# Kernel optimization log

Hardware: AMD Instinct MI355X
Metric: run time of the kernel (lower is better)

The kernel has to match this reference:

```python
import jax, jax.numpy as jnp
import numpy as np

N_NODES = 100000
N_EDGES = 1600000
HIDDEN = 64
N_LAYERS = 3
N_CLASSES = 2
N_GRAPHS = 128
NEG_SLOPE = 0.2  # PyG GATConv default negative_slope


def setup_inputs() -> dict:
    key = jax.random.key(0)
    ks = jax.random.split(key, 8)
    x = jax.random.randint(ks[0], (N_NODES,), 0, 2)
    edge_index = jax.random.randint(ks[1], (2, N_EDGES), 0, N_NODES)
    batch = jnp.sort(jax.random.randint(ks[2], (N_NODES,), 0, N_GRAPHS))
    scale = 1.0 / np.sqrt(HIDDEN)
    embed_table = jax.random.normal(ks[3], (2, HIDDEN), jnp.float32)
    Ws = jax.random.normal(ks[4], (N_LAYERS, HIDDEN, HIDDEN), jnp.float32) * scale
    a_srcs = jax.random.normal(ks[5], (N_LAYERS, HIDDEN), jnp.float32) * scale
    a_dsts = jax.random.normal(ks[6], (N_LAYERS, HIDDEN), jnp.float32) * scale
    biases = jnp.zeros((N_LAYERS, HIDDEN), jnp.float32)
    W_out = jax.random.normal(ks[7], (HIDDEN, N_CLASSES), jnp.float32) * scale
    b_out = jnp.zeros((N_CLASSES,), jnp.float32)
    return {"x": x, "edge_index": edge_index, "batch": batch,
            "embed_table": embed_table, "Ws": Ws, "a_srcs": a_srcs,
            "a_dsts": a_dsts, "biases": biases, "W_out": W_out, "b_out": b_out}


def _gat_layer(h, src, dst, W, a_s, a_d, b):
    # h: [N, D]; src/dst: [E'] (self loops included) -> PyG GATConv, heads=1
    hW = h @ W                                   # [N, D]
    e = jax.nn.leaky_relu((hW @ a_s)[src] + (hW @ a_d)[dst], NEG_SLOPE)  # [E']
    m = jax.ops.segment_max(e, dst, num_segments=N_NODES)               # stable softmax per dst
    ex = jnp.exp(e - m[dst])
    denom = jax.ops.segment_sum(ex, dst, num_segments=N_NODES)
    alpha = ex / denom[dst]                      # [E']
    out = jax.ops.segment_sum(hW[src] * alpha[:, None], dst, num_segments=N_NODES)
    return out + b


def reference(x, edge_index, batch, embed_table, Ws, a_srcs, a_dsts, biases, W_out, b_out):
    loop = jnp.arange(N_NODES)
    src = jnp.concatenate([edge_index[0], loop])  # PyG add_self_loops=True
    dst = jnp.concatenate([edge_index[1], loop])
    h = embed_table[x]                            # [N, D]
    for l in range(N_LAYERS):
        h = _gat_layer(h, src, dst, Ws[l], a_srcs[l], a_dsts[l], biases[l])
        if l < N_LAYERS - 1:
            h = jax.nn.relu(h)
    sums = jax.ops.segment_sum(h, batch, num_segments=N_GRAPHS)
    counts = jax.ops.segment_sum(jnp.ones((N_NODES,), h.dtype), batch, num_segments=N_GRAPHS)
    pooled = sums / jnp.maximum(counts, 1.0)[:, None]  # global_mean_pool
    return pooled @ W_out + b_out                      # [G, num_classes]
```

## Files before the change

### kernel.cpp

```cpp
#include <hip/hip_runtime.h>
#include <hip/hip_bf16.h>
#include <float.h>

#define N_NODES 100000
#define N_EDGES 1600000
#define HIDDEN 64
#define N_GRAPHS 128
#define NEG_SLOPE 0.2f
#define ETOT (N_EDGES + N_NODES)

#define BSHIFT 9
#define NB ((N_NODES + 511) >> BSHIFT)
#define PAIR_CHUNK 4096
#define PAIR_BLOCKS ((N_EDGES + PAIR_CHUNK - 1) / PAIR_CHUNK)
#define XBIT_BLOCKS ((N_NODES + 255) / 256)
#define TBL_BLOCKS (NLVL / 4)

#define NREP 64
#define REP_STRIDE 272
#define NLVL 512

__device__ __forceinline__ unsigned short f2bf(float f) {
    unsigned u = __float_as_uint(f);
    unsigned r = (u + 0x7FFFu + ((u >> 16) & 1u)) >> 16;
    return (unsigned short)r;
}
__device__ __forceinline__ float blo(unsigned u) { return __uint_as_float(u << 16); }
__device__ __forceinline__ float bhi(unsigned u) { return __uint_as_float(u & 0xFFFF0000u); }
__device__ __forceinline__ int sb0(unsigned u) { return (int)((unsigned)(u << 24)) >> 24; }
__device__ __forceinline__ int sb1(unsigned u) { return (int)((unsigned)(u << 16)) >> 24; }
__device__ __forceinline__ int sb2(unsigned u) { return (int)((unsigned)(u << 8)) >> 24; }
__device__ __forceinline__ int sb3(unsigned u) { return (int)u >> 24; }


__global__ __launch_bounds__(256) void k_prep(
    const int* __restrict__ e1, const int* __restrict__ x,
    const float* __restrict__ embed, const float* __restrict__ Ws,
    const float* __restrict__ biases, const float* __restrict__ a_srcs,
    const float* __restrict__ a_dsts, const float* __restrict__ W_out,
    int* __restrict__ blockcnt, float* __restrict__ pool_acc,
    unsigned* __restrict__ xb,
    unsigned char* __restrict__ Tq8, float* __restrict__ Tscl,
    float* __restrict__ Ts1s, float* __restrict__ Ts1d,
    float* __restrict__ sparams)
{
    __shared__ int hcnt[NB];
    int t = threadIdx.x, b = blockIdx.x;

    if (b < PAIR_BLOCKS) {
        if (t < NB) hcnt[t] = 0;
        if (b < NREP && t < 2 * N_GRAPHS) pool_acc[b * REP_STRIDE + t] = 0.f;
        __syncthreads();
        int ebase = b * PAIR_CHUNK;
        int ecount = min(PAIR_CHUNK, N_EDGES - ebase);
        for (int i = t; i < ecount; i += 256)
            atomicAdd(&hcnt[e1[ebase + i] >> BSHIFT], 1);
        __syncthreads();
        if (t < NB) blockcnt[b * NB + t] = hcnt[t];
    } else if (b < PAIR_BLOCKS + TBL_BLOCKS) {
        int l = (b - PAIR_BLOCKS) * 4 + (t >> 6);
        int f = t & 63;
        float r0 = 0.f, r1 = 0.f;
#pragma unroll 8
        for (int k = 0; k < 64; ++k) {
            float w = Ws[k * 64 + f];
            r0 = fmaf(embed[k], w, r0);
            r1 = fmaf(embed[64 + k], w, r1);
        }
        if (l == 0) {
            float as = a_srcs[f], ad = a_dsts[f];
            float t0 = r0 * as, t1 = r1 * as, t2 = r0 * ad, t3 = r1 * ad;
#pragma unroll
            for (int off = 32; off >= 1; off >>= 1) {
                t0 += __shfl_xor(t0, off); t1 += __shfl_xor(t1, off);
                t2 += __shfl_xor(t2, off); t3 += __shfl_xor(t3, off);
            }
            if (f == 0) { sparams[0] = t0; sparams[1] = t1; sparams[2] = t2; sparams[3] = t3; }
        }
        if (l == 1) {
            float b2 = biases[128 + f];
            float t4 = b2 * W_out[f * 2];
            float t5 = b2 * W_out[f * 2 + 1];
#pragma unroll
            for (int off = 32; off >= 1; off >>= 1) {
                t4 += __shfl_xor(t4, off); t5 += __shfl_xor(t5, off);
            }
            if (f == 0) { sparams[4] = t4; sparams[5] = t5; }
        }
        float c1 = (float)l * (1.f / (NLVL - 1));
        float o = fmaxf(biases[f] + r0 + c1 * (r1 - r0), 0.f);
        const float* W1 = Ws + 4096;
        float h = 0.f;
#pragma unroll 8
        for (int k = 0; k < 64; ++k) h = fmaf(__shfl(o, k), W1[k * 64 + f], h);
        float ss = h * a_srcs[64 + f];
        float sd = h * a_dsts[64 + f];
        float am = fabsf(h);
#pragma unroll
        for (int off = 32; off >= 1; off >>= 1) {
            ss += __shfl_xor(ss, off);
            sd += __shfl_xor(sd, off);
            am = fmaxf(am, __shfl_xor(am, off));
        }
        float iscl = (am > 0.f) ? 127.f / am : 0.f;
        Tq8[l * 64 + f] = (unsigned char)(__float2int_rn(h * iscl) & 255);
        if (f == 0) { Tscl[l] = am * (1.f / 127.f); Ts1s[l] = ss; Ts1d[l] = sd; }
    } else {
        int i = (b - PAIR_BLOCKS - TBL_BLOCKS) * 256 + t;
        int lane = t & 63;
        bool bb = (i < N_NODES) && (x[i] != 0);
        unsigned long long m = __ballot(bb);
        int wid = i >> 6;
        if (i < N_NODES + 64) {
            if (lane == 0) xb[wid * 2] = (unsigned)m;
            if (lane == 32) xb[wid * 2 + 1] = (unsigned)(m >> 32);
        }
    }
}

__global__ __launch_bounds__(64) void k_scan_bases(int* __restrict__ blockcnt,
                                                   int* __restrict__ btot) {
    int b = blockIdx.x;
    int lane = threadIdx.x;
    int s = 0;
    for (int base = 0; base < PAIR_BLOCKS; base += 64) {
        int c = base + lane;
        int v = (c < PAIR_BLOCKS) ? blockcnt[c * NB + b] : 0;
        int xv = v;
#pragma unroll
        for (int off = 1; off < 64; off <<= 1) {
            int y = __shfl_up(xv, off);
            if (lane >= off) xv += y;
        }
        if (c < PAIR_BLOCKS) blockcnt[c * NB + b] = s + xv - v;
        s += __shfl(xv, 63);
    }
    if (lane == 0) btot[b] = s;
}

__global__ __launch_bounds__(256) void k_pair_scatter(
    const int* __restrict__ e0, const int* __restrict__ e1,
    const unsigned* __restrict__ xb, const int* __restrict__ btot,
    const int* __restrict__ blockcnt, int* __restrict__ pairs)
{
    __shared__ int tot[256];
    __shared__ int cnt[NB];
    __shared__ int base[NB];
    int t = threadIdx.x, b = blockIdx.x;
    int v = (t < NB) ? btot[t] : 0;
    tot[t] = v;
    __syncthreads();
    for (int off = 1; off < 256; off <<= 1) {
        int u = (t >= off) ? tot[t - off] : 0;
        __syncthreads();
        tot[t] += u;
        __syncthreads();
    }
    if (t < NB) {
        cnt[t] = 0;
        base[t] = (tot[t] - v) + blockcnt[b * NB + t];
    }
    __syncthreads();
    int ebase = b * PAIR_CHUNK;
    int ecount = min(PAIR_CHUNK, N_EDGES - ebase);
    for (int i = t; i < ecount; i += 256) {
        int s = e0[ebase + i];
        int d = e1[ebase + i];
        int xv = (xb[s >> 5] >> (s & 31)) & 1;
        int B = d >> BSHIFT;
        int idx = atomicAdd(&cnt[B], 1);
        pairs[base[B] + idx] = (xv << 26) | ((d & 511) << 17) | s;
    }
}

__global__ __launch_bounds__(512) void k_csr_bucket(
    const int* __restrict__ pairs, const int* __restrict__ btot,
    const int* __restrict__ x, const float* __restrict__ sparams,
    int* __restrict__ rowptr, int* __restrict__ col,
    unsigned short* __restrict__ cidx)
{
    __shared__ int deg[512];
    __shared__ int excl[512];
    __shared__ int cnt2[512];
    __shared__ int wsum[8];
    __shared__ int p0sh;
    int b = blockIdx.x;
    int t = threadIdx.x;
    int nb = b << BSHIFT;
    int nodes = min(512, N_NODES - nb);

    int pv = (t < b) ? btot[t] : 0;
#pragma unroll
    for (int off = 32; off >= 1; off >>= 1) pv += __shfl_xor(pv, off);
    if ((t & 63) == 0) wsum[t >> 6] = pv;
    __syncthreads();
    if (t == 0) {
        int s = 0;
#pragma unroll
        for (int i = 0; i < 8; ++i) s += wsum[i];
        p0sh = s;
    }

    int xself = (t < nodes) ? (x[nb + t] & 1) : 0;
    deg[t] = (t < nodes) ? (1 | (xself << 16)) : 0;
    cnt2[t] = 1;
    __syncthreads();
    int p0 = p0sh;
    int p1 = p0 + btot[b];
    for (int i = p0 + t; i < p1; i += 512) {
        int p = pairs[i];
        atomicAdd(&deg[(p >> 17) & 511], 1 | (((p >> 26) & 1) << 16));
    }
    __syncthreads();

    int packed = deg[t];
    int val = packed & 0xFFFF;
    int kx = packed >> 16;
    if (t < nodes) {
        float ss0 = sparams[0], ss1 = sparams[1];
        float sd = xself ? sparams[3] : sparams[2];
        float e0 = ss0 + sd; e0 = (e0 >= 0.f) ? e0 : NEG_SLOPE * e0;
        float e1 = ss1 + sd; e1 = (e1 >= 0.f) ? e1 : NEG_SLOPE * e1;
        float pp0 = __expf(e0), pp1 = __expf(e1);
        float kn = (float)kx, dn = (float)(val - kx);
        float c1 = kn * pp1 / (dn * pp0 + kn * pp1);
        cidx[nb + t] = (unsigned short)__float2int_rn(c1 * (float)(NLVL - 1));
    }

    int xx = val;
#pragma unroll
    for (int off = 1; off < 64; off <<= 1) {
        int y = __shfl_up(xx, off);
        if ((t & 63) >= off) xx += y;
    }
    __syncthreads();
    if ((t & 63) == 63) wsum[t >> 6] = xx;
    __syncthreads();
    if (t == 0) {
        int s = 0;
#pragma unroll
        for (int i = 0; i < 8; ++i) { int v = wsum[i]; wsum[i] = s; s += v; }
    }
    __syncthreads();
    int ex = xx - val + wsum[t >> 6];
    excl[t] = ex;

    int colbase = p0 + nb;
    if (t < nodes) {
        rowptr[nb + t] = colbase + ex;
        col[colbase + ex] = nb + t;
    }
    if (b == NB - 1 && t == 0) rowptr[N_NODES] = ETOT;
    __syncthreads();
    for (int i = p0 + t; i < p1; i += 512) {
        int p = pairs[i];
        int li = (p >> 17) & 511;
        int pos = colbase + excl[li] + atomicAdd(&cnt2[li], 1);
        col[pos] = p & 0x1FFFF;
    }
}


__global__ __launch_bounds__(256) void k_agg1(
    const unsigned char* __restrict__ Tq8, const float* __restrict__ Tscl,
    const float* __restrict__ Ts1s, const float* __restrict__ Ts1d,
    const unsigned short* __restrict__ cidx, const int* __restrict__ col,
    const int* __restrict__ rowptr, const float* __restrict__ bias,
    unsigned short* __restrict__ hout)
{
    __shared__ float2 stash[4][64];
    int t = threadIdx.x;
    int wave = t >> 6, lane = t & 63;
    int h = lane >> 5, hl = lane & 31;
    int base = blockIdx.x * 8 + wave * 2;
    if (base >= N_NODES) return;
    const char* hb = (const char*)Tq8;

    int node = base + h;
    bool valid = (node < N_NODES);
    int row = 0, end = 0;
    if (valid) { row = rowptr[node]; end = rowptr[node + 1]; }
    int deg = end - row;
    int degO = __shfl_xor(deg, 32);
    bool fast = (deg <= 32) && (degO <= 32);

    if (fast) {
        int idx = 0;
        float p = 0.f, sc = 0.f;
        if (hl < deg) idx = cidx[col[row + hl]];
        float sdi = Ts1d[__shfl(idx, h * 32)];
        if (hl < deg) {
            float ee = Ts1s[idx] + sdi;
            ee = (ee >= 0.f) ? ee : NEG_SLOPE * ee;
            p = __expf(ee);
            sc = Tscl[idx];
        }
        stash[wave][lane] = make_float2(p * sc, __int_as_float(idx * 64));

        int q = hl >> 4;
        int f = hl & 15;
        int f4 = f * 4;
        int sb = h * 32;
        float a0 = 0.f, a1 = 0.f, a2 = 0.f, a3 = 0.f;
        int degr = (deg + 7) & ~7;
        for (int j = q; j < degr; j += 8) {
            float2 e0 = stash[wave][sb + j];
            float2 e1 = stash[wave][sb + j + 2];
            float2 e2 = stash[wave][sb + j + 4];
            float2 e3 = stash[wave][sb + j + 6];
            unsigned v0 = *(const unsigned*)(hb + (__float_as_int(e0.y) + f4));
            unsigned v1 = *(const unsigned*)(hb + (__float_as_int(e1.y) + f4));
            unsigned v2 = *(const unsigned*)(hb + (__float_as_int(e2.y) + f4));
            unsigned v3 = *(const unsigned*)(hb + (__float_as_int(e3.y) + f4));
            a0 = fmaf(e0.x, (float)sb0(v0), a0);
            a1 = fmaf(e0.x, (float)sb1(v0), a1);
            a2 = fmaf(e0.x, (float)sb2(v0), a2);
            a3 = fmaf(e0.x, (float)sb3(v0), a3);
            a0 = fmaf(e1.x, (float)sb0(v1), a0);
            a1 = fmaf(e1.x, (float)sb1(v1), a1);
            a2 = fmaf(e1.x, (float)sb2(v1), a2);
            a3 = fmaf(e1.x, (float)sb3(v1), a3);
            a0 = fmaf(e2.x, (float)sb0(v2), a0);
            a1 = fmaf(e2.x, (float)sb1(v2), a1);
            a2 = fmaf(e2.x, (float)sb2(v2), a2);
            a3 = fmaf(e2.x, (float)sb3(v2), a3);
            a0 = fmaf(e3.x, (float)sb0(v3), a0);
            a1 = fmaf(e3.x, (float)sb1(v3), a1);
            a2 = fmaf(e3.x, (float)sb2(v3), a2);
            a3 = fmaf(e3.x, (float)sb3(v3), a3);
        }
        float denom = p;
#pragma unroll
        for (int off = 16; off >= 1; off >>= 1) denom += __shfl_xor(denom, off);
        float inv = 1.f / denom;
        a0 += __shfl_xor(a0, 16);
        a1 += __shfl_xor(a1, 16);
        a2 += __shfl_xor(a2, 16);
        a3 += __shfl_xor(a3, 16);
        if (hl < 16 && valid) {
            float4 bb = *(const float4*)&bias[4 * f];
            ushort4 pk;
            pk.x = f2bf(fmaxf(fmaf(a0, inv, bb.x), 0.f));
            pk.y = f2bf(fmaxf(fmaf(a1, inv, bb.y), 0.f));
            pk.z = f2bf(fmaxf(fmaf(a2, inv, bb.z), 0.f));
            pk.w = f2bf(fmaxf(fmaf(a3, inv, bb.w), 0.f));
            *(ushort4*)&hout[node * 64 + 4 * f] = pk;
        }
    } else {
        for (int s = 0; s < 2; ++s) {
            int nd = base + s;
            if (nd >= N_NODES) continue;
            int r = rowptr[nd], e = rowptr[nd + 1];
            float sdi = Ts1d[cidx[nd]];
            float m = -FLT_MAX;
            for (int j = r + lane; j < e; j += 64) {
                float ee = Ts1s[cidx[col[j]]] + sdi;
                ee = (ee >= 0.f) ? ee : NEG_SLOPE * ee;
                m = fmaxf(m, ee);
            }
#pragma unroll
            for (int off = 32; off >= 1; off >>= 1) m = fmaxf(m, __shfl_xor(m, off));
            float denom = 0.f;
            for (int j = r + lane; j < e; j += 64) {
                float ee = Ts1s[cidx[col[j]]] + sdi;
                ee = (ee >= 0.f) ? ee : NEG_SLOPE * ee;
                denom += __expf(ee - m);
            }
#pragma unroll
            for (int off = 32; off >= 1; off >>= 1) denom += __shfl_xor(denom, off);
            float inv = 1.f / denom;
            float acc = 0.f;
            for (int j = r; j < e; ++j) {
                int idxj = cidx[col[j]];
                float ee = Ts1s[idxj] + sdi;
                ee = (ee >= 0.f) ? ee : NEG_SLOPE * ee;
                float w = __expf(ee - m) * inv * Tscl[idxj];
                int bq = (int)(signed char)Tq8[idxj * 64 + lane];
                acc = fmaf(w, (float)bq, acc);
            }
            hout[nd * 64 + lane] = f2bf(fmaxf(acc + bias[lane], 0.f));
        }
    }
}


__global__ __launch_bounds__(256) void k_gemm2(
    const unsigned* __restrict__ h32, const float* __restrict__ W,
    const float* __restrict__ a_s, const float* __restrict__ a_d,
    const float* __restrict__ W_out,
    float2* __restrict__ z2, float* __restrict__ s_src, float* __restrict__ s_dst)
{
    __shared__ float Wl[64 * 64];
    __shared__ float hT[64 * 68];
    int t = threadIdx.x;
    int r0 = blockIdx.x * 64;

    for (int i = t; i < 4096; i += 256) Wl[i] = W[i];
    for (int i = t; i < 2048; i += 256) {
        int r = i >> 5, m = i & 31;
        int row = r0 + r;
        unsigned u = (row < N_NODES) ? h32[row * 32 + m] : 0u;
        hT[(2 * m) * 68 + r]     = blo(u);
        hT[(2 * m + 1) * 68 + r] = bhi(u);
    }
    __syncthreads();

    int tcol = t & 15;
    int trow = t >> 4;
    float acc[4][4];
#pragma unroll
    for (int i = 0; i < 4; ++i)
#pragma unroll
        for (int j = 0; j < 4; ++j) acc[i][j] = 0.f;

    for (int k = 0; k < 64; ++k) {
        float4 va = *(const float4*)&hT[k * 68 + trow * 4];
        float4 vb = *(const float4*)&Wl[k * 64 + tcol * 4];
        float a[4] = {va.x, va.y, va.z, va.w};
        float bb[4] = {vb.x, vb.y, vb.z, vb.w};
#pragma unroll
        for (int i = 0; i < 4; ++i)
#pragma unroll
            for (int j = 0; j < 4; ++j) acc[i][j] = fmaf(a[i], bb[j], acc[i][j]);
    }

    float4 as4 = *(const float4*)&a_s[tcol * 4];
    float4 ad4 = *(const float4*)&a_d[tcol * 4];
    float asr[4] = {as4.x, as4.y, as4.z, as4.w};
    float adr[4] = {ad4.x, ad4.y, ad4.z, ad4.w};
    float4 wa = *(const float4*)&W_out[8 * tcol];
    float4 wb = *(const float4*)&W_out[8 * tcol + 4];

#pragma unroll
    for (int i = 0; i < 4; ++i) {
        int row = r0 + trow * 4 + i;
        float ps = 0.f, pd = 0.f;
#pragma unroll
        for (int j = 0; j < 4; ++j) {
            ps = fmaf(acc[i][j], asr[j], ps);
            pd = fmaf(acc[i][j], adr[j], pd);
        }
        float z0 = acc[i][0] * wa.x + acc[i][1] * wa.z + acc[i][2] * wb.x + acc[i][3] * wb.z;
        float z1 = acc[i][0] * wa.y + acc[i][1] * wa.w + acc[i][2] * wb.y + acc[i][3] * wb.w;
#pragma unroll
        for (int off = 8; off >= 1; off >>= 1) {
            ps += __shfl_xor(ps, off);
            pd += __shfl_xor(pd, off);
            z0 += __shfl_xor(z0, off);
            z1 += __shfl_xor(z1, off);
        }
        if (row < N_NODES && tcol == 0) {
            s_src[row] = ps; s_dst[row] = pd;
            z2[row] = make_float2(z0, z1);
        }
    }
}


__global__ __launch_bounds__(256) void k_pool2(
    const float2* __restrict__ z2, const int* __restrict__ col,
    const int* __restrict__ rowptr, const float* __restrict__ s_src_in,
    const float* __restrict__ s_dst_in, const int* __restrict__ batch,
    float* __restrict__ pool_acc)
{
    int t = threadIdx.x;
    int wave = t >> 6, lane = t & 63;
    int h = lane >> 5, hl = lane & 31;
    int base0 = blockIdx.x * 32 + wave * 8;
    if (base0 >= N_NODES) return;
    float* rep = pool_acc + ((blockIdx.x * 4 + wave) & (NREP - 1)) * REP_STRIDE;

    int gcur = -1;
    float acc0 = 0.f, acc1 = 0.f;

#pragma unroll
    for (int i = 0; i < 4; ++i) {
        int node = base0 + 2 * i + h;
        bool valid = (node < N_NODES);
        int row = 0, end = 0;
        if (valid) { row = rowptr[node]; end = rowptr[node + 1]; }
        int deg = end - row;
        int degO = __shfl_xor(deg, 32);
        bool fast = (deg <= 32) && (degO <= 32);
        float r0 = 0.f, r1 = 0.f;

        if (fast) {
            float sdi = valid ? s_dst_in[node] : 0.f;
            float p = 0.f;
            float2 zv = make_float2(0.f, 0.f);
            if (hl < deg) {
                int c = col[row + hl];
                float ee = s_src_in[c] + sdi;
                ee = (ee >= 0.f) ? ee : NEG_SLOPE * ee;
                p = __expf(ee);
                zv = z2[c];
            }
            float n0 = p * zv.x, n1 = p * zv.y, dn = p;
#pragma unroll
            for (int off = 16; off >= 1; off >>= 1) {
                n0 += __shfl_xor(n0, off);
                n1 += __shfl_xor(n1, off);
                dn += __shfl_xor(dn, off);
            }
            float inv = 1.f / dn;
            r0 = n0 * inv; r1 = n1 * inv;
        } else {
            float rr0[2], rr1[2];
#pragma unroll
            for (int s = 0; s < 2; ++s) {
                rr0[s] = rr1[s] = 0.f;
                int nd = base0 + 2 * i + s;
                if (nd >= N_NODES) continue;
                int r = rowptr[nd], e = rowptr[nd + 1];
                float sdi = s_dst_in[nd];
                float n0 = 0.f, n1 = 0.f, dn = 0.f;
                for (int j = r + lane; j < e; j += 64) {
                    int c = col[j];
                    float ee = s_src_in[c] + sdi;
                    ee = (ee >= 0.f) ? ee : NEG_SLOPE * ee;
                    float p = __expf(ee);
                    float2 zv = z2[c];
                    n0 = fmaf(p, zv.x, n0);
                    n1 = fmaf(p, zv.y, n1);
                    dn += p;
                }
#pragma unroll
                for (int off = 32; off >= 1; off >>= 1) {
                    n0 += __shfl_xor(n0, off);
                    n1 += __shfl_xor(n1, off);
                    dn += __shfl_xor(dn, off);
                }
                float inv = 1.f / dn;
                rr0[s] = n0 * inv; rr1[s] = n1 * inv;
            }
            r0 = rr0[h]; r1 = rr1[h];
        }

        if (hl == 0 && valid) {
            int g = batch[node];
            if (g != gcur) {
                if (gcur >= 0) {
                    atomicAdd(&rep[gcur * 2], acc0);
                    atomicAdd(&rep[gcur * 2 + 1], acc1);
                }
                gcur = g; acc0 = r0; acc1 = r1;
            } else {
                acc0 += r0; acc1 += r1;
            }
        }
    }
    if (hl == 0 && gcur >= 0) {
        atomicAdd(&rep[gcur * 2], acc0);
        atomicAdd(&rep[gcur * 2 + 1], acc1);
    }
}


__device__ __forceinline__ int lower_bound_dev(const int* __restrict__ a, int n, int v) {
    int lo = 0, hi = n;
    while (lo < hi) {
        int mid = (lo + hi) >> 1;
        if (a[mid] < v) lo = mid + 1; else hi = mid;
    }
    return lo;
}

__global__ void k_head(const float* __restrict__ pool_acc,
                       const int* __restrict__ batch,
                       const float* __restrict__ b_out,
                       const float* __restrict__ sparams,
                       float* __restrict__ out)
{
    int t = threadIdx.x;
    if (t < 2 * N_GRAPHS) {
        float s = 0.f;
#pragma unroll 8
        for (int r = 0; r < NREP; ++r) s += pool_acc[r * REP_STRIDE + t];
        int g = t >> 1, c = t & 1;
        int start = lower_bound_dev(batch, N_NODES, g);
        int end = lower_bound_dev(batch, N_NODES, g + 1);
        float cnt = fmaxf((float)(end - start), 1.f);
        out[t] = s / cnt + sparams[4 + c] + b_out[c];
    }
}


extern "C" void kernel_launch(void* const* d_in, const int* in_sizes, int n_in,
                              void* d_out, int out_size, void* d_ws, size_t ws_size,
                              hipStream_t stream) {
    const int*   x       = (const int*)d_in[0];
    const int*   edge    = (const int*)d_in[1];
    const int*   batch   = (const int*)d_in[2];
    const float* embed   = (const float*)d_in[3];
    const float* Ws      = (const float*)d_in[4];
    const float* a_srcs  = (const float*)d_in[5];
    const float* a_dsts  = (const float*)d_in[6];
    const float* biases  = (const float*)d_in[7];
    const float* W_out   = (const float*)d_in[8];
    const float* b_out   = (const float*)d_in[9];
    float* out = (float*)d_out;

    char* ws = (char*)d_ws;
    size_t off = 0;
    auto alloc = [&](size_t bytes) -> void* {
        void* p = ws + off;
        off += (bytes + 255) & ~(size_t)255;
        return p;
    };
    unsigned short* hout  = (unsigned short*)alloc((size_t)N_NODES * 64 * sizeof(unsigned short));
    float2* z2      = (float2*)alloc((size_t)N_NODES * sizeof(float2));
    float* s_src0   = (float*)alloc((size_t)N_NODES * sizeof(float));
    float* s_dst0   = (float*)alloc((size_t)N_NODES * sizeof(float));
    unsigned short* cidx = (unsigned short*)alloc((size_t)N_NODES * sizeof(unsigned short));
    int*   rowptr   = (int*)alloc((size_t)(N_NODES + 1) * sizeof(int));
    int*   colA     = (int*)alloc((size_t)ETOT * sizeof(int));
    int*   blockcnt = (int*)alloc((size_t)PAIR_BLOCKS * NB * sizeof(int));
    int*   btot     = (int*)alloc((size_t)NB * sizeof(int));
    float* pool_acc = (float*)alloc((size_t)(NREP * REP_STRIDE) * sizeof(float));
    unsigned* xb    = (unsigned*)alloc((size_t)3232 * sizeof(unsigned));
    unsigned char* Tq8 = (unsigned char*)alloc((size_t)NLVL * 64);
    float* Tscl     = (float*)alloc((size_t)NLVL * sizeof(float));
    float* Ts1s     = (float*)alloc((size_t)NLVL * sizeof(float));
    float* Ts1d     = (float*)alloc((size_t)NLVL * sizeof(float));
    float* sparams  = (float*)alloc((size_t)8 * sizeof(float));
    int*   pairs    = (int*)alloc((size_t)N_EDGES * sizeof(int));

    const int* e0 = edge;
    const int* e1 = edge + N_EDGES;

    k_prep<<<PAIR_BLOCKS + TBL_BLOCKS + XBIT_BLOCKS, 256, 0, stream>>>(
        e1, x, embed, Ws, biases, a_srcs, a_dsts, W_out,
        blockcnt, pool_acc, xb, Tq8, Tscl, Ts1s, Ts1d, sparams);
    k_scan_bases<<<NB, 64, 0, stream>>>(blockcnt, btot);
    k_pair_scatter<<<PAIR_BLOCKS, 256, 0, stream>>>(e0, e1, xb, btot, blockcnt, pairs);
    k_csr_bucket<<<NB, 512, 0, stream>>>(pairs, btot, x, sparams, rowptr, colA, cidx);

    k_agg1<<<(N_NODES + 7) / 8, 256, 0, stream>>>(
        Tq8, Tscl, Ts1s, Ts1d, cidx, colA, rowptr, biases + 64, hout);
    k_gemm2<<<(N_NODES + 63) / 64, 256, 0, stream>>>(
        (const unsigned*)hout, Ws + 8192, a_srcs + 128, a_dsts + 128, W_out,
        z2, s_src0, s_dst0);
    k_pool2<<<(N_NODES + 31) / 32, 256, 0, stream>>>(
        z2, colA, rowptr, s_src0, s_dst0, batch, pool_acc);
    k_head<<<1, 256, 0, stream>>>(pool_acc, batch, b_out, sparams, out);
}
```

Measured before the change: 213.7 us.

## Count degrees with global atomics in scatter and use smaller CSR buckets

Per-destination degree counting moves out of the bucket CSR kernel into the pair-scatter kernel, which now does a global atomicAdd per edge into a zeroed degg array. The bucket size shrinks from 512 to 256 nodes, doubling the bucket count (NB about 391), and the block sizes of the scatter and CSR kernels are swapped to match. The goal is to drop one full pass over the pairs array in k_csr_bucket and to get more, smaller CSR blocks for better parallelism. In exchange it adds 1.6M global atomics and larger per-block histograms and scans.

```diff
diff --git a/kernel.cpp b/kernel.cpp
--- a/kernel.cpp
+++ b/kernel.cpp
@@ -9,8 +9,8 @@
 #define NEG_SLOPE 0.2f
 #define ETOT (N_EDGES + N_NODES)
 
-#define BSHIFT 9
-#define NB ((N_NODES + 511) >> BSHIFT)
+#define BSHIFT 8
+#define NB ((N_NODES + 255) >> BSHIFT)
 #define PAIR_CHUNK 4096
 #define PAIR_BLOCKS ((N_EDGES + PAIR_CHUNK - 1) / PAIR_CHUNK)
 #define XBIT_BLOCKS ((N_NODES + 255) / 256)
@@ -39,7 +39,7 @@
     const float* __restrict__ biases, const float* __restrict__ a_srcs,
     const float* __restrict__ a_dsts, const float* __restrict__ W_out,
     int* __restrict__ blockcnt, float* __restrict__ pool_acc,
-    unsigned* __restrict__ xb,
+    unsigned* __restrict__ xb, int* __restrict__ degg,
     unsigned char* __restrict__ Tq8, float* __restrict__ Tscl,
     float* __restrict__ Ts1s, float* __restrict__ Ts1d,
     float* __restrict__ sparams)
@@ -48,7 +48,7 @@
     int t = threadIdx.x, b = blockIdx.x;
 
     if (b < PAIR_BLOCKS) {
-        if (t < NB) hcnt[t] = 0;
+        for (int i = t; i < NB; i += 256) hcnt[i] = 0;
         if (b < NREP && t < 2 * N_GRAPHS) pool_acc[b * REP_STRIDE + t] = 0.f;
         __syncthreads();
         int ebase = b * PAIR_CHUNK;
@@ -56,7 +56,7 @@
         for (int i = t; i < ecount; i += 256)
             atomicAdd(&hcnt[e1[ebase + i] >> BSHIFT], 1);
         __syncthreads();
-        if (t < NB) blockcnt[b * NB + t] = hcnt[t];
+        for (int i = t; i < NB; i += 256) blockcnt[b * NB + i] = hcnt[i];
     } else if (b < PAIR_BLOCKS + TBL_BLOCKS) {
         int l = (b - PAIR_BLOCKS) * 4 + (t >> 6);
         int f = t & 63;
@@ -115,6 +115,7 @@
             if (lane == 0) xb[wid * 2] = (unsigned)m;
             if (lane == 32) xb[wid * 2 + 1] = (unsigned)(m >> 32);
         }
+        if (i < N_NODES) degg[i] = 0;
     }
 }
 
@@ -138,19 +139,20 @@
     if (lane == 0) btot[b] = s;
 }
 
-__global__ __launch_bounds__(256) void k_pair_scatter(
+__global__ __launch_bounds__(512) void k_pair_scatter(
     const int* __restrict__ e0, const int* __restrict__ e1,
     const unsigned* __restrict__ xb, const int* __restrict__ btot,
-    const int* __restrict__ blockcnt, int* __restrict__ pairs)
+    const int* __restrict__ blockcnt, int* __restrict__ degg,
+    int* __restrict__ pairs)
 {
-    __shared__ int tot[256];
+    __shared__ int tot[512];
     __shared__ int cnt[NB];
     __shared__ int base[NB];
     int t = threadIdx.x, b = blockIdx.x;
     int v = (t < NB) ? btot[t] : 0;
     tot[t] = v;
     __syncthreads();
-    for (int off = 1; off < 256; off <<= 1) {
+    for (int off = 1; off < 512; off <<= 1) {
         int u = (t >= off) ? tot[t - off] : 0;
         __syncthreads();
         tot[t] += u;
@@ -163,57 +165,48 @@
     __syncthreads();
     int ebase = b * PAIR_CHUNK;
     int ecount = min(PAIR_CHUNK, N_EDGES - ebase);
-    for (int i = t; i < ecount; i += 256) {
+    for (int i = t; i < ecount; i += 512) {
         int s = e0[ebase + i];
         int d = e1[ebase + i];
         int xv = (xb[s >> 5] >> (s & 31)) & 1;
+        atomicAdd(&degg[d], 1 | (xv << 16));
         int B = d >> BSHIFT;
         int idx = atomicAdd(&cnt[B], 1);
-        pairs[base[B] + idx] = (xv << 26) | ((d & 511) << 17) | s;
-    }
-}
-
-__global__ __launch_bounds__(512) void k_csr_bucket(
+        pairs[base[B] + idx] = (xv << 25) | ((d & 255) << 17) | s;
+    }
+}
+
+__global__ __launch_bounds__(256) void k_csr_bucket(
     const int* __restrict__ pairs, const int* __restrict__ btot,
-    const int* __restrict__ x, const float* __restrict__ sparams,
+    const int* __restrict__ x, const int* __restrict__ degg,
+    const float* __restrict__ sparams,
     int* __restrict__ rowptr, int* __restrict__ col,
     unsigned short* __restrict__ cidx)
 {
-    __shared__ int deg[512];
-    __shared__ int excl[512];
-    __shared__ int cnt2[512];
-    __shared__ int wsum[8];
+    __shared__ int excl[256];
+    __shared__ int cnt2[256];
+    __shared__ int wsum[4];
     __shared__ int p0sh;
     int b = blockIdx.x;
     int t = threadIdx.x;
     int nb = b << BSHIFT;
-    int nodes = min(512, N_NODES - nb);
+    int nodes = min(256, N_NODES - nb);
 
     int pv = (t < b) ? btot[t] : 0;
+    if (t + 256 < b) pv += btot[t + 256];
 #pragma unroll
     for (int off = 32; off >= 1; off >>= 1) pv += __shfl_xor(pv, off);
     if ((t & 63) == 0) wsum[t >> 6] = pv;
     __syncthreads();
-    if (t == 0) {
-        int s = 0;
-#pragma unroll
-        for (int i = 0; i < 8; ++i) s += wsum[i];
-        p0sh = s;
-    }
+    if (t == 0) p0sh = wsum[0] + wsum[1] + wsum[2] + wsum[3];
 
     int xself = (t < nodes) ? (x[nb + t] & 1) : 0;
-    deg[t] = (t < nodes) ? (1 | (xself << 16)) : 0;
+    int packed = ((t < nodes) ? degg[nb + t] : 0) + ((t < nodes) ? (1 | (xself << 16)) : 0);
     cnt2[t] = 1;
     __syncthreads();
     int p0 = p0sh;
     int p1 = p0 + btot[b];
-    for (int i = p0 + t; i < p1; i += 512) {
-        int p = pairs[i];
-        atomicAdd(&deg[(p >> 17) & 511], 1 | (((p >> 26) & 1) << 16));
-    }
-    __syncthreads();
-
-    int packed = deg[t];
+
     int val = packed & 0xFFFF;
     int kx = packed >> 16;
     if (t < nodes) {
@@ -239,7 +232,7 @@
     if (t == 0) {
         int s = 0;
 #pragma unroll
-        for (int i = 0; i < 8; ++i) { int v = wsum[i]; wsum[i] = s; s += v; }
+        for (int i = 0; i < 4; ++i) { int v = wsum[i]; wsum[i] = s; s += v; }
     }
     __syncthreads();
     int ex = xx - val + wsum[t >> 6];
@@ -252,9 +245,9 @@
     }
     if (b == NB - 1 && t == 0) rowptr[N_NODES] = ETOT;
     __syncthreads();
-    for (int i = p0 + t; i < p1; i += 512) {
+    for (int i = p0 + t; i < p1; i += 256) {
         int p = pairs[i];
-        int li = (p >> 17) & 511;
+        int li = (p >> 17) & 255;
         int pos = colbase + excl[li] + atomicAdd(&cnt2[li], 1);
         col[pos] = p & 0x1FFFF;
     }
@@ -612,6 +605,7 @@
     float* s_src0   = (float*)alloc((size_t)N_NODES * sizeof(float));
     float* s_dst0   = (float*)alloc((size_t)N_NODES * sizeof(float));
     unsigned short* cidx = (unsigned short*)alloc((size_t)N_NODES * sizeof(unsigned short));
+    int*   degg     = (int*)alloc((size_t)N_NODES * sizeof(int));
     int*   rowptr   = (int*)alloc((size_t)(N_NODES + 1) * sizeof(int));
     int*   colA     = (int*)alloc((size_t)ETOT * sizeof(int));
     int*   blockcnt = (int*)alloc((size_t)PAIR_BLOCKS * NB * sizeof(int));
@@ -630,10 +624,10 @@
 
     k_prep<<<PAIR_BLOCKS + TBL_BLOCKS + XBIT_BLOCKS, 256, 0, stream>>>(
         e1, x, embed, Ws, biases, a_srcs, a_dsts, W_out,
-        blockcnt, pool_acc, xb, Tq8, Tscl, Ts1s, Ts1d, sparams);
+        blockcnt, pool_acc, xb, degg, Tq8, Tscl, Ts1s, Ts1d, sparams);
     k_scan_bases<<<NB, 64, 0, stream>>>(blockcnt, btot);
-    k_pair_scatter<<<PAIR_BLOCKS, 256, 0, stream>>>(e0, e1, xb, btot, blockcnt, pairs);
-    k_csr_bucket<<<NB, 512, 0, stream>>>(pairs, btot, x, sparams, rowptr, colA, cidx);
+    k_pair_scatter<<<PAIR_BLOCKS, 512, 0, stream>>>(e0, e1, xb, btot, blockcnt, degg, pairs);
+    k_csr_bucket<<<NB, 256, 0, stream>>>(pairs, btot, x, degg, sparams, rowptr, colA, cidx);
 
     k_agg1<<<(N_NODES + 7) / 8, 256, 0, stream>>>(
         Tq8, Tscl, Ts1s, Ts1d, cidx, colA, rowptr, biases + 64, hout);
```

After: 266.5 us. +24.7%, slower.
